# Optimization experiments

Measured on AMD Instinct MI355X. Metric: run time of the kernel, lower is better.

Reference implementation:

```python
import jax, jax.numpy as jnp
import numpy as np

KEEP_PROB = 0.8  # dropout_keep_probability from settings


def setup_inputs() -> dict:
    key = jax.random.key(0)
    ks = jax.random.split(key, 7)
    N, E, D_IN, D_OUT = 100000, 600000, 128, 128
    x = jax.random.normal(ks[0], (N, D_IN), dtype=jnp.float32)
    W_f = jax.random.normal(ks[1], (D_IN, D_OUT), dtype=jnp.float32) * (1.0 / np.sqrt(D_IN))
    W_b = jax.random.normal(ks[2], (D_IN, D_OUT), dtype=jnp.float32) * (1.0 / np.sqrt(D_IN))
    W_s = jax.random.normal(ks[3], (D_IN, D_OUT), dtype=jnp.float32) * (1.0 / np.sqrt(D_IN))
    drop_u = jax.random.uniform(ks[4], (N, D_OUT), dtype=jnp.float32)
    senders = jax.random.randint(ks[5], (E,), 0, N, dtype=jnp.int64)
    receivers = jax.random.randint(ks[6], (E,), 0, N, dtype=jnp.int64)
    return {"x": x, "W_f": W_f, "W_b": W_b, "W_s": W_s,
            "drop_u": drop_u, "senders": senders, "receivers": receivers}


def reference(x, W_f, W_b, W_s, drop_u, senders, receivers):
    N = x.shape[0]
    # gather vertex features for each edge endpoint (embedding_lookup)
    sender_feats = x[senders]      # [E, d_in]
    receiver_feats = x[receivers]  # [E, d_in]
    # compute_messages: per-direction linear transforms
    forward_messages = sender_feats @ W_f    # [E, d_out]
    backward_messages = receiver_feats @ W_b  # [E, d_out]
    # self-loop messages with dropout (train mode), inverted-dropout scaling
    keep_mask = (drop_u < KEEP_PROB).astype(x.dtype) / KEEP_PROB
    self_loop = (x @ W_s) * keep_mask  # [N, d_out]
    # combine_messages: scatter-sum forward msgs to receivers, backward to senders
    agg = (jax.ops.segment_sum(forward_messages, receivers, num_segments=N)
           + jax.ops.segment_sum(backward_messages, senders, num_segments=N)
           + self_loop)
    # use_nonlinearity=True
    return jax.nn.relu(agg)
```

## Files before the change

### kernel.cpp

```cpp
#include <hip/hip_runtime.h>

typedef float fvec4 __attribute__((ext_vector_type(4)));
typedef float f32x4 __attribute__((ext_vector_type(4)));
typedef short bf16x8 __attribute__((ext_vector_type(8)));

#define D   128
#define CAP 32

static __device__ __forceinline__ unsigned bcu(float f) {
    return __builtin_bit_cast(unsigned, f);
}
static __device__ __forceinline__ unsigned pack_bf2(float f0, float f1) {
    unsigned a0 = bcu(f0) + 0x8000u;
    unsigned a1 = bcu(f1) + 0x8000u;
    return __builtin_amdgcn_perm(a1, a0, 0x07060302u);
}
static __device__ __forceinline__ unsigned short f2bf_rne(float f) {
    unsigned u = bcu(f);
    u += 0x7FFFu + ((u >> 16) & 1u);
    return (unsigned short)(u >> 16);
}

__global__ __launch_bounds__(256) void prep_w(
    const float* __restrict__ Wf, const float* __restrict__ Wb,
    const float* __restrict__ Ws, unsigned short* __restrict__ Wsw)
{
    int t = blockIdx.x * 256 + threadIdx.x;
    if (t >= 3 * 128 * 128) return;
    int p   = t >> 14;
    int e   = t & 16383;
    int row = e >> 7;
    int c   = e & 127;
    int u   = (c >> 3) ^ (row & 15);
    int k   = u * 8 + (c & 7);
    const float* W = (p == 0) ? Ws : (p == 1) ? Wf : Wb;
    Wsw[t] = f2bf_rne(W[k * D + row]);
}

__global__ __launch_bounds__(256) void conv_fill(
    const float* __restrict__ x, unsigned short* __restrict__ xb,
    const int* __restrict__ send, const int* __restrict__ recv,
    int* __restrict__ counts, int* __restrict__ adj,
    int N, int E, int Nfill)
{
    const int bid = blockIdx.x;
    if (bid < Nfill) {
        int t = bid * 256 + threadIdx.x;
        int e = t >> 1;
        if (e < E) {
            int c, src;
            if (t & 1) { c = recv[e];     src = send[e]; }
            else       { c = N + send[e]; src = recv[e]; }
            int pos = atomicAdd(counts + c, 1);
            if (pos < CAP) adj[(size_t)c * CAP + pos] = src;
        }
        return;
    }
    size_t base = ((size_t)(bid - Nfill) * 256 + threadIdx.x) * 8;
    if (base >= (size_t)N * D) return;
    fvec4 a = *(const fvec4*)(x + base);
    fvec4 b = *(const fvec4*)(x + base + 4);
    uint4 p;
    p.x = pack_bf2(a[0], a[1]);
    p.y = pack_bf2(a[2], a[3]);
    p.z = pack_bf2(b[0], b[1]);
    p.w = pack_bf2(b[2], b[3]);
    *(uint4*)(xb + base) = p;
}

static __device__ __forceinline__ float bflo(unsigned u) {
    return __builtin_bit_cast(float, u << 16);
}
static __device__ __forceinline__ float bfhi(unsigned u) {
    return __builtin_bit_cast(float, u & 0xFFFF0000u);
}

__global__ __launch_bounds__(256) void gather_S(
    const unsigned short* __restrict__ xb, const int* __restrict__ counts,
    const int* __restrict__ adj, unsigned short* __restrict__ S, int N)
{
    const int wave = threadIdx.x >> 6;
    const int v = blockIdx.x * 4 + wave;
    if (v >= N) return;
    const int lane = threadIdx.x & 63;
    const int grp = lane >> 4;
    const int l16 = lane & 15;

    float acc[2][8];
#pragma unroll
    for (int d = 0; d < 2; ++d)
#pragma unroll
        for (int i = 0; i < 8; ++i) acc[d][i] = 0.0f;

#pragma unroll
    for (int d = 0; d < 2; ++d) {
        const int cv = d ? (N + v) : v;
        int deg = counts[cv];
        if (deg > CAP) deg = CAP;
        const int* ap = adj + (size_t)cv * CAP;
        float* a = acc[d];

        int j = grp;
        for (; j + 4 < deg; j += 8) {
            int i0 = ap[j], i1 = ap[j + 4];
            uint4 u0 = *(const uint4*)(xb + (size_t)i0 * D + l16 * 8);
            uint4 u1 = *(const uint4*)(xb + (size_t)i1 * D + l16 * 8);
            a[0] += bflo(u0.x); a[1] += bfhi(u0.x);
            a[2] += bflo(u0.y); a[3] += bfhi(u0.y);
            a[4] += bflo(u0.z); a[5] += bfhi(u0.z);
            a[6] += bflo(u0.w); a[7] += bfhi(u0.w);
            a[0] += bflo(u1.x); a[1] += bfhi(u1.x);
            a[2] += bflo(u1.y); a[3] += bfhi(u1.y);
            a[4] += bflo(u1.z); a[5] += bfhi(u1.z);
            a[6] += bflo(u1.w); a[7] += bfhi(u1.w);
        }
        if (j < deg) {
            int i0 = ap[j];
            uint4 u0 = *(const uint4*)(xb + (size_t)i0 * D + l16 * 8);
            a[0] += bflo(u0.x); a[1] += bfhi(u0.x);
            a[2] += bflo(u0.y); a[3] += bfhi(u0.y);
            a[4] += bflo(u0.z); a[5] += bfhi(u0.z);
            a[6] += bflo(u0.w); a[7] += bfhi(u0.w);
        }
    }

#pragma unroll
    for (int i = 0; i < 8; ++i) {
        acc[0][i] += __shfl_xor(acc[0][i], 16, 64);
        acc[0][i] += __shfl_xor(acc[0][i], 32, 64);
        acc[1][i] += __shfl_xor(acc[1][i], 16, 64);
        acc[1][i] += __shfl_xor(acc[1][i], 32, 64);
    }

    float f0, f1, b0, b1;
    if (grp == 0)      { f0 = acc[0][0]; f1 = acc[0][1]; b0 = acc[1][0]; b1 = acc[1][1]; }
    else if (grp == 1) { f0 = acc[0][2]; f1 = acc[0][3]; b0 = acc[1][2]; b1 = acc[1][3]; }
    else if (grp == 2) { f0 = acc[0][4]; f1 = acc[0][5]; b0 = acc[1][4]; b1 = acc[1][5]; }
    else               { f0 = acc[0][6]; f1 = acc[0][7]; b0 = acc[1][6]; b1 = acc[1][7]; }

    unsigned short* Sp = S + (size_t)v * 256 + l16 * 8 + grp * 2;
    *(unsigned*)Sp         = pack_bf2(f0, f1);
    *(unsigned*)(Sp + 128) = pack_bf2(b0, b1);
}

__global__ __launch_bounds__(256, 4) void gemm_out(
    const unsigned short* __restrict__ xb,
    const unsigned short* __restrict__ Sm,
    const unsigned short* __restrict__ Wsw,
    const float* __restrict__ drop_u,
    float* __restrict__ out, int N)
{
    __shared__ unsigned short ldsW[128 * 128];

    const int wave = threadIdx.x >> 6;
    const int lane = threadIdx.x & 63;
    const int quad = lane >> 4;
    const int m16  = lane & 15;
    const int row  = blockIdx.x * 64 + wave * 16 + m16;
    const int rowc = (row < N) ? row : N - 1;

    auto stage = [&](int p) {
        const char* src = (const char*)(Wsw + (size_t)p * 16384);
#pragma unroll
        for (int r = 0; r < 8; ++r) {
            const int unit = r * 256 + wave * 64;
            __builtin_amdgcn_global_load_lds(
                (const __attribute__((address_space(1))) unsigned*)
                    (src + (size_t)(unit + lane) * 16),
                (__attribute__((address_space(3))) unsigned*)
                    ((char*)ldsW + (size_t)unit * 16),
                16, 0, 0);
        }
    };

    stage(0);

    const unsigned short* xp = xb + (size_t)rowc * D;
    bf16x8 xf[4];
#pragma unroll
    for (int kc = 0; kc < 4; ++kc)
        xf[kc] = *(const bf16x8*)(xp + kc * 32 + quad * 8);
    fvec4 u[8];
#pragma unroll
    for (int ct = 0; ct < 8; ++ct)
        u[ct] = *(const fvec4*)(drop_u + (size_t)rowc * D + ct * 16 + quad * 4);

    f32x4 C[8];
#pragma unroll
    for (int ct = 0; ct < 8; ++ct) C[ct] = (f32x4){0.f, 0.f, 0.f, 0.f};

    auto mfma_pass = [&]() {
#pragma unroll
        for (int kc = 0; kc < 4; ++kc) {
#pragma unroll
            for (int ct = 0; ct < 8; ++ct) {
                const unsigned short* wp =
                    ldsW + (size_t)(ct * 16 + m16) * 128 +
                    (((kc * 4 + quad) ^ m16) * 8);
                bf16x8 wf = *(const bf16x8*)wp;
                C[ct] = __builtin_amdgcn_mfma_f32_16x16x32_bf16(
                    wf, xf[kc], C[ct], 0, 0, 0);
            }
        }
    };

    __syncthreads();
    mfma_pass();
    __syncthreads();
    stage(1);

#pragma unroll
    for (int ct = 0; ct < 8; ++ct) {
#pragma unroll
        for (int c = 0; c < 4; ++c)
            C[ct][c] *= (u[ct][c] < 0.8f) ? 1.25f : 0.0f;
    }
    const unsigned short* sp = Sm + (size_t)rowc * 256;
#pragma unroll
    for (int kc = 0; kc < 4; ++kc)
        xf[kc] = *(const bf16x8*)(sp + kc * 32 + quad * 8);

    __syncthreads();
    mfma_pass();
    __syncthreads();
    stage(2);

#pragma unroll
    for (int kc = 0; kc < 4; ++kc)
        xf[kc] = *(const bf16x8*)(sp + 128 + kc * 32 + quad * 8);

    __syncthreads();
    mfma_pass();

    if (row < N) {
#pragma unroll
        for (int ct = 0; ct < 8; ++ct) {
            fvec4 r;
#pragma unroll
            for (int c = 0; c < 4; ++c)
                r[c] = fmaxf(C[ct][c], 0.0f);
            *(fvec4*)(out + (size_t)row * D + ct * 16 + quad * 4) = r;
        }
    }
}

extern "C" void kernel_launch(void* const* d_in, const int* in_sizes, int n_in,
                              void* d_out, int out_size, void* d_ws, size_t ws_size,
                              hipStream_t stream)
{
    const float* x      = (const float*)d_in[0];
    const float* W_f    = (const float*)d_in[1];
    const float* W_b    = (const float*)d_in[2];
    const float* W_s    = (const float*)d_in[3];
    const float* drop_u = (const float*)d_in[4];
    const int*   send   = (const int*)d_in[5];
    const int*   recv   = (const int*)d_in[6];

    const int N = in_sizes[0] / D;
    const int E = in_sizes[5];

    float* out = (float*)d_out;

    unsigned short* Wsw = (unsigned short*)d_ws;
    unsigned short* xb  = Wsw + (size_t)3 * 128 * 128;
    unsigned short* Sm  = xb + (size_t)N * D;
    int* counts = (int*)(Sm + (size_t)N * 256);
    int* adj    = counts + (size_t)2 * N;

    const int Nfill = (2 * E + 255) / 256;
    const int Nconv = (N * D + 2047) / 2048;
    const int Nb    = (N + 63) / 64;

    prep_w<<<(3 * 128 * 128 + 255) / 256, 256, 0, stream>>>(W_f, W_b, W_s, Wsw);

    hipMemsetAsync(counts, 0, (size_t)2 * N * sizeof(int), stream);

    conv_fill<<<Nfill + Nconv, 256, 0, stream>>>(x, xb, send, recv,
                                                 counts, adj, N, E, Nfill);

    gather_S<<<(N + 3) / 4, 256, 0, stream>>>(xb, counts, adj, Sm, N);

    gemm_out<<<Nb, 256, 0, stream>>>(xb, Sm, Wsw, drop_u, out, N);
}
```

Measured before the change: 323.1 us.

## Fuse neighbor gather into GEMM kernel and process both edge directions per thread

```diff
diff --git a/kernel.cpp b/kernel.cpp
--- a/kernel.cpp
+++ b/kernel.cpp
@@ -19,6 +19,12 @@
     unsigned u = bcu(f);
     u += 0x7FFFu + ((u >> 16) & 1u);
     return (unsigned short)(u >> 16);
+}
+static __device__ __forceinline__ float bflo(unsigned u) {
+    return __builtin_bit_cast(float, u << 16);
+}
+static __device__ __forceinline__ float bfhi(unsigned u) {
+    return __builtin_bit_cast(float, u & 0xFFFF0000u);
 }
 
 __global__ __launch_bounds__(256) void prep_w(
@@ -45,14 +51,14 @@
 {
     const int bid = blockIdx.x;
     if (bid < Nfill) {
-        int t = bid * 256 + threadIdx.x;
-        int e = t >> 1;
+        int e = bid * 256 + threadIdx.x;
         if (e < E) {
-            int c, src;
-            if (t & 1) { c = recv[e];     src = send[e]; }
-            else       { c = N + send[e]; src = recv[e]; }
-            int pos = atomicAdd(counts + c, 1);
-            if (pos < CAP) adj[(size_t)c * CAP + pos] = src;
+            int s = send[e];
+            int r = recv[e];
+            int p0 = atomicAdd(counts + r, 1);
+            int p1 = atomicAdd(counts + N + s, 1);
+            if (p0 < CAP) adj[(size_t)r * CAP + p0] = s;
+            if (p1 < CAP) adj[((size_t)(N + s)) * CAP + p1] = r;
         }
         return;
     }
@@ -68,86 +74,11 @@
     *(uint4*)(xb + base) = p;
 }
 
-static __device__ __forceinline__ float bflo(unsigned u) {
-    return __builtin_bit_cast(float, u << 16);
-}
-static __device__ __forceinline__ float bfhi(unsigned u) {
-    return __builtin_bit_cast(float, u & 0xFFFF0000u);
-}
-
-__global__ __launch_bounds__(256) void gather_S(
-    const unsigned short* __restrict__ xb, const int* __restrict__ counts,
-    const int* __restrict__ adj, unsigned short* __restrict__ S, int N)
-{
-    const int wave = threadIdx.x >> 6;
-    const int v = blockIdx.x * 4 + wave;
-    if (v >= N) return;
-    const int lane = threadIdx.x & 63;
-    const int grp = lane >> 4;
-    const int l16 = lane & 15;
-
-    float acc[2][8];
-#pragma unroll
-    for (int d = 0; d < 2; ++d)
-#pragma unroll
-        for (int i = 0; i < 8; ++i) acc[d][i] = 0.0f;
-
-#pragma unroll
-    for (int d = 0; d < 2; ++d) {
-        const int cv = d ? (N + v) : v;
-        int deg = counts[cv];
-        if (deg > CAP) deg = CAP;
-        const int* ap = adj + (size_t)cv * CAP;
-        float* a = acc[d];
-
-        int j = grp;
-        for (; j + 4 < deg; j += 8) {
-            int i0 = ap[j], i1 = ap[j + 4];
-            uint4 u0 = *(const uint4*)(xb + (size_t)i0 * D + l16 * 8);
-            uint4 u1 = *(const uint4*)(xb + (size_t)i1 * D + l16 * 8);
-            a[0] += bflo(u0.x); a[1] += bfhi(u0.x);
-            a[2] += bflo(u0.y); a[3] += bfhi(u0.y);
-            a[4] += bflo(u0.z); a[5] += bfhi(u0.z);
-            a[6] += bflo(u0.w); a[7] += bfhi(u0.w);
-            a[0] += bflo(u1.x); a[1] += bfhi(u1.x);
-            a[2] += bflo(u1.y); a[3] += bfhi(u1.y);
-            a[4] += bflo(u1.z); a[5] += bfhi(u1.z);
-            a[6] += bflo(u1.w); a[7] += bfhi(u1.w);
-        }
-        if (j < deg) {
-            int i0 = ap[j];
-            uint4 u0 = *(const uint4*)(xb + (size_t)i0 * D + l16 * 8);
-            a[0] += bflo(u0.x); a[1] += bfhi(u0.x);
-            a[2] += bflo(u0.y); a[3] += bfhi(u0.y);
-            a[4] += bflo(u0.z); a[5] += bfhi(u0.z);
-            a[6] += bflo(u0.w); a[7] += bfhi(u0.w);
-        }
-    }
-
-#pragma unroll
-    for (int i = 0; i < 8; ++i) {
-        acc[0][i] += __shfl_xor(acc[0][i], 16, 64);
-        acc[0][i] += __shfl_xor(acc[0][i], 32, 64);
-        acc[1][i] += __shfl_xor(acc[1][i], 16, 64);
-        acc[1][i] += __shfl_xor(acc[1][i], 32, 64);
-    }
-
-    float f0, f1, b0, b1;
-    if (grp == 0)      { f0 = acc[0][0]; f1 = acc[0][1]; b0 = acc[1][0]; b1 = acc[1][1]; }
-    else if (grp == 1) { f0 = acc[0][2]; f1 = acc[0][3]; b0 = acc[1][2]; b1 = acc[1][3]; }
-    else if (grp == 2) { f0 = acc[0][4]; f1 = acc[0][5]; b0 = acc[1][4]; b1 = acc[1][5]; }
-    else               { f0 = acc[0][6]; f1 = acc[0][7]; b0 = acc[1][6]; b1 = acc[1][7]; }
-
-    unsigned short* Sp = S + (size_t)v * 256 + l16 * 8 + grp * 2;
-    *(unsigned*)Sp         = pack_bf2(f0, f1);
-    *(unsigned*)(Sp + 128) = pack_bf2(b0, b1);
-}
-
-__global__ __launch_bounds__(256, 4) void gemm_out(
+__global__ __launch_bounds__(256, 4) void gemm_fused(
     const unsigned short* __restrict__ xb,
-    const unsigned short* __restrict__ Sm,
     const unsigned short* __restrict__ Wsw,
     const float* __restrict__ drop_u,
+    const int* __restrict__ counts, const int* __restrict__ adj,
     float* __restrict__ out, int N)
 {
     __shared__ unsigned short ldsW[128 * 128];
@@ -180,10 +111,6 @@
 #pragma unroll
     for (int kc = 0; kc < 4; ++kc)
         xf[kc] = *(const bf16x8*)(xp + kc * 32 + quad * 8);
-    fvec4 u[8];
-#pragma unroll
-    for (int ct = 0; ct < 8; ++ct)
-        u[ct] = *(const fvec4*)(drop_u + (size_t)rowc * D + ct * 16 + quad * 4);
 
     f32x4 C[8];
 #pragma unroll
@@ -204,30 +131,91 @@
         }
     };
 
+    auto gather_dir = [&](int base) {
+        float s[4][8];
+#pragma unroll
+        for (int kc = 0; kc < 4; ++kc)
+#pragma unroll
+            for (int i = 0; i < 8; ++i) s[kc][i] = 0.0f;
+
+        const int cv = base + rowc;
+        int deg = counts[cv];
+        if (deg > CAP) deg = CAP;
+        const int* ap = adj + (size_t)cv * CAP;
+
+        auto accum = [&](int src) {
+            const unsigned short* sp = xb + (size_t)src * D + quad * 8;
+            uint4 v0 = *(const uint4*)(sp);
+            uint4 v1 = *(const uint4*)(sp + 32);
+            uint4 v2 = *(const uint4*)(sp + 64);
+            uint4 v3 = *(const uint4*)(sp + 96);
+            s[0][0] += bflo(v0.x); s[0][1] += bfhi(v0.x);
+            s[0][2] += bflo(v0.y); s[0][3] += bfhi(v0.y);
+            s[0][4] += bflo(v0.z); s[0][5] += bfhi(v0.z);
+            s[0][6] += bflo(v0.w); s[0][7] += bfhi(v0.w);
+            s[1][0] += bflo(v1.x); s[1][1] += bfhi(v1.x);
+            s[1][2] += bflo(v1.y); s[1][3] += bfhi(v1.y);
+            s[1][4] += bflo(v1.z); s[1][5] += bfhi(v1.z);
+            s[1][6] += bflo(v1.w); s[1][7] += bfhi(v1.w);
+            s[2][0] += bflo(v2.x); s[2][1] += bfhi(v2.x);
+            s[2][2] += bflo(v2.y); s[2][3] += bfhi(v2.y);
+            s[2][4] += bflo(v2.z); s[2][5] += bfhi(v2.z);
+            s[2][6] += bflo(v2.w); s[2][7] += bfhi(v2.w);
+            s[3][0] += bflo(v3.x); s[3][1] += bfhi(v3.x);
+            s[3][2] += bflo(v3.y); s[3][3] += bfhi(v3.y);
+            s[3][4] += bflo(v3.z); s[3][5] += bfhi(v3.z);
+            s[3][6] += bflo(v3.w); s[3][7] += bfhi(v3.w);
+        };
+
+        int s0 = (0 < deg) ? ap[0] : 0;
+        int s1 = (1 < deg) ? ap[1] : 0;
+        int j = 0;
+        while (__any(j < deg)) {
+            int n0 = (j + 2 < deg) ? ap[j + 2] : 0;
+            int n1 = (j + 3 < deg) ? ap[j + 3] : 0;
+            if (j < deg)     accum(s0);
+            if (j + 1 < deg) accum(s1);
+            s0 = n0; s1 = n1;
+            j += 2;
+        }
+
+#pragma unroll
+        for (int kc = 0; kc < 4; ++kc) {
+            uint4 p;
+            p.x = pack_bf2(s[kc][0], s[kc][1]);
+            p.y = pack_bf2(s[kc][2], s[kc][3]);
+            p.z = pack_bf2(s[kc][4], s[kc][5]);
+            p.w = pack_bf2(s[kc][6], s[kc][7]);
+            xf[kc] = __builtin_bit_cast(bf16x8, p);
+        }
+    };
+
     __syncthreads();
     mfma_pass();
     __syncthreads();
     stage(1);
 
-#pragma unroll
-    for (int ct = 0; ct < 8; ++ct) {
-#pragma unroll
-        for (int c = 0; c < 4; ++c)
-            C[ct][c] *= (u[ct][c] < 0.8f) ? 1.25f : 0.0f;
+    {
+        fvec4 u[8];
+#pragma unroll
+        for (int ct = 0; ct < 8; ++ct)
+            u[ct] = *(const fvec4*)(drop_u + (size_t)rowc * D + ct * 16 + quad * 4);
+#pragma unroll
+        for (int ct = 0; ct < 8; ++ct) {
+#pragma unroll
+            for (int c = 0; c < 4; ++c)
+                C[ct][c] *= (u[ct][c] < 0.8f) ? 1.25f : 0.0f;
+        }
     }
-    const unsigned short* sp = Sm + (size_t)rowc * 256;
-#pragma unroll
-    for (int kc = 0; kc < 4; ++kc)
-        xf[kc] = *(const bf16x8*)(sp + kc * 32 + quad * 8);
+
+    gather_dir(0);
 
     __syncthreads();
     mfma_pass();
     __syncthreads();
     stage(2);
 
-#pragma unroll
-    for (int kc = 0; kc < 4; ++kc)
-        xf[kc] = *(const bf16x8*)(sp + 128 + kc * 32 + quad * 8);
+    gather_dir(N);
 
     __syncthreads();
     mfma_pass();
@@ -263,11 +251,10 @@
 
     unsigned short* Wsw = (unsigned short*)d_ws;
     unsigned short* xb  = Wsw + (size_t)3 * 128 * 128;
-    unsigned short* Sm  = xb + (size_t)N * D;
-    int* counts = (int*)(Sm + (size_t)N * 256);
+    int* counts = (int*)(xb + (size_t)N * D);
     int* adj    = counts + (size_t)2 * N;
 
-    const int Nfill = (2 * E + 255) / 256;
+    const int Nfill = (E + 255) / 256;
     const int Nconv = (N * D + 2047) / 2048;
     const int Nb    = (N + 63) / 64;
 
@@ -278,7 +265,5 @@
     conv_fill<<<Nfill + Nconv, 256, 0, stream>>>(x, xb, send, recv,
                                                  counts, adj, N, E, Nfill);
 
-    gather_S<<<(N + 3) / 4, 256, 0, stream>>>(xb, counts, adj, Sm, N);
-
-    gemm_out<<<Nb, 256, 0, stream>>>(xb, Sm, Wsw, drop_u, out, N);
-}
+    gemm_fused<<<Nb, 256, 0, stream>>>(xb, Wsw, drop_u, counts, adj, out, N);
+}
```

After: 356.6 us. 10.4% more time.
